# Kernel tuning notes

Measured on AMD Instinct MI355X. Metric: run time of the kernel, lower is better.

Reference implementation:

```python
import jax, jax.numpy as jnp
from jax import lax
import numpy as np


def _lstm_layer(x, Wih, Whh, bih, bhh):
    """Single-direction LSTM layer, PyTorch gate order (i, f, g, o).
    x: [B, T, D_in] -> hidden sequence [B, T, H]."""
    B, T, _ = x.shape
    H = Whh.shape[1]
    # Precompute input contribution for all timesteps: [B, T, 4H]
    xw = jnp.einsum('btd,gd->btg', x, Wih) + bih + bhh

    def step(carry, xt):
        h, c = carry
        gates = xt + h @ Whh.T  # [B, 4H]
        i, f, g, o = jnp.split(gates, 4, axis=-1)
        i = jax.nn.sigmoid(i)
        f = jax.nn.sigmoid(f)
        g = jnp.tanh(g)
        o = jax.nn.sigmoid(o)
        c = f * c + i * g
        h = o * jnp.tanh(c)
        return (h, c), h

    h0 = jnp.zeros((B, H), dtype=x.dtype)
    c0 = jnp.zeros((B, H), dtype=x.dtype)
    _, hs = lax.scan(step, (h0, c0), jnp.swapaxes(xw, 0, 1))  # [T, B, H]
    return jnp.swapaxes(hs, 0, 1)  # [B, T, H]


def setup_inputs() -> dict:
    key = jax.random.key(0)
    ks = jax.random.split(key, 9)
    B, T, D, H = 64, 2048, 256, 128
    s = 1.0 / np.sqrt(H)  # PyTorch uniform(-1/sqrt(H), 1/sqrt(H)) init scale
    u = lambda k, shp: jax.random.uniform(k, shp, jnp.float32, -s, s)
    return {
        'x': jax.random.normal(ks[0], (B, T, D), jnp.float32),
        'Wih0': u(ks[1], (4 * H, D)),
        'Whh0': u(ks[2], (4 * H, H)),
        'bih0': u(ks[3], (4 * H,)),
        'bhh0': u(ks[4], (4 * H,)),
        'Wih1': u(ks[5], (4 * H, H)),
        'Whh1': u(ks[6], (4 * H, H)),
        'bih1': u(ks[7], (4 * H,)),
        'bhh1': u(ks[8], (4 * H,)),
    }


def reference(x, Wih0, Whh0, bih0, bhh0, Wih1, Whh1, bih1, bhh1):
    # 2-layer stacked LSTM; inter-layer dropout (p=0.1) is identity at eval.
    h1 = _lstm_layer(x, Wih0, Whh0, bih0, bhh0)
    h2 = _lstm_layer(h1, Wih1, Whh1, bih1, bhh1)
    return h2
```

## Files before the change

### kernel.cpp

```cpp
#include <hip/hip_runtime.h>
#include <hip/hip_bf16.h>

#define H 128
#define FOURH 512
#define BATCH 64
#define SEQ 2048
#define TC SEQ
#define NCHUNK 128
#define NGEMMB 224

typedef _Float16 half8 __attribute__((ext_vector_type(8)));
typedef float f32x4 __attribute__((ext_vector_type(4)));

__global__ void prep_kernel(const float* __restrict__ Wih0,
                            const float* __restrict__ bih0, const float* __restrict__ bhh0,
                            const float* __restrict__ bih1, const float* __restrict__ bhh1,
                            float* __restrict__ Wt0,
                            float* __restrict__ b0, float* __restrict__ b1,
                            int* __restrict__ flags) {
    int id = blockIdx.x * 256 + threadIdx.x;
    const int N0 = 256 * 512;
    if (id < N0) {
        int k = id >> 9, n = id & 511;
        Wt0[id] = Wih0[n * 256 + k];
    } else if (id < N0 + 512) {
        int i = id - N0;
        b0[i] = bih0[i] + bhh0[i];
    } else if (id < N0 + 1024) {
        int i = id - (N0 + 512);
        b1[i] = bih1[i] + bhh1[i];
    } else if (id < N0 + 1024 + 8 + NCHUNK) {
        flags[id - (N0 + 1024)] = 0;
    }
}

__device__ __forceinline__ float sigmoid_f(float x) {
    return __builtin_amdgcn_rcpf(1.f + __expf(-x));
}
__device__ __forceinline__ float tanh_f(float x) {
    return 1.f - 2.f * __builtin_amdgcn_rcpf(__expf(2.f * x) + 1.f);
}

#define LDS_BARRIER()                                                \
    do {                                                             \
        asm volatile("s_waitcnt lgkmcnt(0)" ::: "memory");           \
        __builtin_amdgcn_s_barrier();                                \
        __builtin_amdgcn_sched_barrier(0);                           \
    } while (0)

#define BM 128
#define BN 128
#define BK 32

__global__ __launch_bounds__(512, 2) void lstm_fused_kernel(
    const float* __restrict__ x,
    const float* __restrict__ Wt0,
    const float* __restrict__ b0sum,
    float* __restrict__ G,
    const float* __restrict__ Whh0,
    const float* __restrict__ Wih1,
    const float* __restrict__ Whh1,
    const float* __restrict__ b1,
    _Float16* __restrict__ h1p,
    float* __restrict__ out,
    int* __restrict__ flags)
{
    const int tid = threadIdx.x;

    int* prodF     = flags;
    int* chunkDone = flags + 8;

    __shared__ _Float16 hbuf[2][8][136];
    __shared__ float As[BK][BM + 4];
    __shared__ float Bs[BK][BN];

    if (blockIdx.x >= 16) {
        const int j   = blockIdx.x - 16;
        const int sub = j & 31;
        const int cls = j >> 5;
        const int by  = sub >> 2;
        const int bx  = sub & 3;
        const int n0  = bx * BN;
        const int tm  = tid >> 5;
        const int tn  = tid & 31;

        int ar[2], aq[2], bkk[2], bq[2];
#pragma unroll
        for (int l = 0; l < 2; ++l) {
            int fidx = tid + l * 512;
            ar[l] = fidx >> 3; aq[l] = fidx & 7;
            bkk[l] = fidx >> 5; bq[l] = fidx & 31;
        }
        float4 bv = *(const float4*)&b0sum[n0 + tn * 4];

        for (int c = cls; c < NCHUNK; c += 7) {
            const float* aptr[2];
#pragma unroll
            for (int l = 0; l < 2; ++l) {
                int rl = by * BM + ar[l];
                int b = rl >> 4;
                int t = c * 16 + (rl & 15);
                aptr[l] = x + ((size_t)b * SEQ + t) * 256 + aq[l] * 4;
            }
            float acc[2][4][4];
#pragma unroll
            for (int rh = 0; rh < 2; ++rh)
#pragma unroll
                for (int i = 0; i < 4; ++i)
#pragma unroll
                    for (int jj = 0; jj < 4; ++jj) acc[rh][i][jj] = 0.f;

            for (int k0 = 0; k0 < 256; k0 += BK) {
                __syncthreads();
#pragma unroll
                for (int l = 0; l < 2; ++l) {
                    float4 v = *(const float4*)(aptr[l] + k0);
                    As[aq[l] * 4 + 0][ar[l]] = v.x;
                    As[aq[l] * 4 + 1][ar[l]] = v.y;
                    As[aq[l] * 4 + 2][ar[l]] = v.z;
                    As[aq[l] * 4 + 3][ar[l]] = v.w;
                }
#pragma unroll
                for (int l = 0; l < 2; ++l) {
                    float4 v = *(const float4*)(Wt0 + (size_t)(k0 + bkk[l]) * FOURH + n0 + bq[l] * 4);
                    *(float4*)&Bs[bkk[l]][bq[l] * 4] = v;
                }
                __syncthreads();
#pragma unroll
                for (int kk = 0; kk < BK; ++kk) {
                    float a[8], bb[4];
                    *(float4*)&a[0] = *(const float4*)&As[kk][tm * 4];
                    *(float4*)&a[4] = *(const float4*)&As[kk][64 + tm * 4];
                    *(float4*)&bb[0] = *(const float4*)&Bs[kk][tn * 4];
#pragma unroll
                    for (int rh = 0; rh < 2; ++rh)
#pragma unroll
                        for (int i = 0; i < 4; ++i)
#pragma unroll
                            for (int jj = 0; jj < 4; ++jj)
                                acc[rh][i][jj] = fmaf(a[rh * 4 + i], bb[jj], acc[rh][i][jj]);
                }
            }
#pragma unroll
            for (int rh = 0; rh < 2; ++rh)
#pragma unroll
                for (int i = 0; i < 4; ++i) {
                    int rl = by * BM + rh * 64 + tm * 4 + i;
                    int b = rl >> 4;
                    int t = c * 16 + (rl & 15);
                    float* gp = G + ((size_t)b * SEQ + t) * FOURH + n0 + tn * 4;
                    float4 o = make_float4(acc[rh][i][0] + bv.x, acc[rh][i][1] + bv.y,
                                           acc[rh][i][2] + bv.z, acc[rh][i][3] + bv.w);
                    *(float4*)gp = o;
                }
            __syncthreads();
            if (tid == 0) {
                __threadfence();
                __hip_atomic_fetch_add(&chunkDone[c], 1, __ATOMIC_RELEASE,
                                       __HIP_MEMORY_SCOPE_AGENT);
            }
        }
        return;
    }

    const int w  = tid >> 6;
    const int l  = tid & 63;
    const int li = l & 15;
    const int q  = l >> 4;
    const int u  = 16 * w + li;
    const int b0 = q * 2;
    const int ab = ((li >> 2) * 2) + (li & 1);

#define WAIT_FLAG(ptr, tgtv)                                                   \
    do {                                                                       \
        if (tid == 0) {                                                        \
            while (__hip_atomic_load((ptr), __ATOMIC_RELAXED,                  \
                                     __HIP_MEMORY_SCOPE_AGENT) < (tgtv))       \
                __builtin_amdgcn_s_sleep(4);                                   \
            (void)__hip_atomic_load((ptr), __ATOMIC_ACQUIRE,                   \
                                    __HIP_MEMORY_SCOPE_AGENT);                 \
        }                                                                      \
        __syncthreads();                                                       \
    } while (0)

    if (blockIdx.x < 8) {
        const int g = blockIdx.x;

        half8 Bf[4][4];
#pragma unroll
        for (int tl = 0; tl < 4; ++tl)
#pragma unroll
            for (int kf = 0; kf < 4; ++kf) {
                const float* wp = Whh0 + (size_t)(tl * 128 + u) * H + kf * 32 + q * 8;
                float4 v0 = *(const float4*)wp;
                float4 v1 = *(const float4*)(wp + 4);
                half8 b;
                b[0] = (_Float16)v0.x; b[1] = (_Float16)v0.y;
                b[2] = (_Float16)v0.z; b[3] = (_Float16)v0.w;
                b[4] = (_Float16)v1.x; b[5] = (_Float16)v1.y;
                b[6] = (_Float16)v1.z; b[7] = (_Float16)v1.w;
                Bf[tl][kf] = b;
            }

        float c0 = 0.f, c1 = 0.f, h0 = 0.f, h1v = 0.f;
        hbuf[0][b0][u]     = (_Float16)0.f;
        hbuf[0][b0 + 1][u] = (_Float16)0.f;

        const float* gb = G + (size_t)(8 * g) * TC * FOURH;
        const int voff0 = b0 * TC * FOURH + u;
        const int voff1 = (b0 + 1) * TC * FOURH + u;

        WAIT_FLAG(&chunkDone[0], 32);

        float G0[8], G1[8], G2[8], G3[8];
        const float* gld = gb;
#pragma unroll
        for (int tl = 0; tl < 4; ++tl) {
            G0[tl * 2 + 0] = gld[voff0 + tl * H];
            G0[tl * 2 + 1] = gld[voff1 + tl * H];
        }
        gld += FOURH;
#pragma unroll
        for (int tl = 0; tl < 4; ++tl) {
            G1[tl * 2 + 0] = gld[voff0 + tl * H];
            G1[tl * 2 + 1] = gld[voff1 + tl * H];
        }
        gld += FOURH;
#pragma unroll
        for (int tl = 0; tl < 4; ++tl) {
            G2[tl * 2 + 0] = gld[voff0 + tl * H];
            G2[tl * 2 + 1] = gld[voff1 + tl * H];
        }
        gld += FOURH;
#pragma unroll
        for (int tl = 0; tl < 4; ++tl) {
            G3[tl * 2 + 0] = gld[voff0 + tl * H];
            G3[tl * 2 + 1] = gld[voff1 + tl * H];
        }
        gld += FOURH;

        _Float16* php = h1p + (size_t)(8 * g + b0) * H + u;

#define P_STEP(PB, GR)                                                            \
    {                                                                             \
        half8 Afr[4];                                                             \
        _Pragma("unroll")                                                         \
        for (int kf = 0; kf < 4; ++kf)                                            \
            Afr[kf] = *(const half8*)&hbuf[PB][ab][kf * 32 + q * 8];              \
        f32x4 acc[4];                                                             \
        _Pragma("unroll")                                                         \
        for (int tl = 0; tl < 4; ++tl) {                                          \
            acc[tl][0] = GR[tl * 2 + 0]; acc[tl][1] = GR[tl * 2 + 1];             \
            acc[tl][2] = 0.f;            acc[tl][3] = 0.f;                        \
        }                                                                         \
        _Pragma("unroll")                                                         \
        for (int tl = 0; tl < 4; ++tl) {                                          \
            GR[tl * 2 + 0] = gld[voff0 + tl * H];                                 \
            GR[tl * 2 + 1] = gld[voff1 + tl * H];                                 \
        }                                                                         \
        gld += FOURH;                                                             \
        _Pragma("unroll")                                                         \
        for (int kf = 0; kf < 4; ++kf)                                            \
            _Pragma("unroll")                                                     \
            for (int tl = 0; tl < 4; ++tl)                                        \
                acc[tl] = __builtin_amdgcn_mfma_f32_16x16x32_f16(Afr[kf], Bf[tl][kf], acc[tl], 0, 0, 0); \
        {                                                                         \
            float ig = sigmoid_f(acc[0][0]);                                      \
            float fg = sigmoid_f(acc[1][0]);                                      \
            float gg = tanh_f(acc[2][0]);                                         \
            float og = sigmoid_f(acc[3][0]);                                      \
            c0 = fmaf(fg, c0, ig * gg);                                           \
            h0 = og * tanh_f(c0);                                                 \
            float ig1 = sigmoid_f(acc[0][1]);                                     \
            float fg1 = sigmoid_f(acc[1][1]);                                     \
            float gg1 = tanh_f(acc[2][1]);                                        \
            float og1 = sigmoid_f(acc[3][1]);                                     \
            c1 = fmaf(fg1, c1, ig1 * gg1);                                        \
            h1v = og1 * tanh_f(c1);                                               \
        }                                                                         \
        hbuf[PB ^ 1][b0][u]     = (_Float16)h0;                                   \
        hbuf[PB ^ 1][b0 + 1][u] = (_Float16)h1v;                                  \
        php[0]   = (_Float16)h0;                                                  \
        php[128] = (_Float16)h1v;                                                 \
        php += BATCH * H;                                                         \
        LDS_BARRIER();                                                            \
    }

        for (int s4 = 0; s4 < TC; s4 += 4) {
            if ((s4 & 15) == 0) {
                int k = (s4 >> 4) + 1;
                if (k > NCHUNK - 1) k = NCHUNK - 1;
                WAIT_FLAG(&chunkDone[k], 32);
            }
            P_STEP(0, G0)
            P_STEP(1, G1)
            P_STEP(0, G2)
            P_STEP(1, G3)
            if ((s4 & 31) == 28) {
                __threadfence();
                __syncthreads();
                if (tid == 0)
                    __hip_atomic_store(&prodF[g], s4 + 4, __ATOMIC_RELEASE,
                                       __HIP_MEMORY_SCOPE_AGENT);
            }
        }
#undef P_STEP
    } else {
        const int g = blockIdx.x - 8;

        half8 Bf[4][8];
#pragma unroll
        for (int tl = 0; tl < 4; ++tl)
#pragma unroll
            for (int kf = 0; kf < 8; ++kf) {
                const float* base = (kf < 4) ? Wih1 : Whh1;
                int kk = (kf & 3) * 32 + q * 8;
                const float* wp = base + (size_t)(tl * 128 + u) * H + kk;
                float4 v0 = *(const float4*)wp;
                float4 v1 = *(const float4*)(wp + 4);
                half8 b;
                b[0] = (_Float16)v0.x; b[1] = (_Float16)v0.y;
                b[2] = (_Float16)v0.z; b[3] = (_Float16)v0.w;
                b[4] = (_Float16)v1.x; b[5] = (_Float16)v1.y;
                b[6] = (_Float16)v1.z; b[7] = (_Float16)v1.w;
                Bf[tl][kf] = b;
            }

        float bv[4];
#pragma unroll
        for (int tl = 0; tl < 4; ++tl) bv[tl] = b1[tl * 128 + u];

        float c0 = 0.f, c1 = 0.f, h0, h1v;
        hbuf[0][b0][u]     = (_Float16)0.f;
        hbuf[0][b0 + 1][u] = (_Float16)0.f;

        const _Float16* h1pG = h1p + (size_t)(8 * g + ab) * H + q * 8;
        float* op0 = out + (size_t)(8 * g + b0) * SEQ * H + u;
        float* op1 = out + (size_t)(8 * g + b0 + 1) * SEQ * H + u;

        WAIT_FLAG(&prodF[g], 64);

        half8 Af0[4], Af1[4];
#pragma unroll
        for (int kf = 0; kf < 4; ++kf)
            Af0[kf] = *(const half8*)(h1pG + kf * 32);
        {
            const _Float16* hp = h1pG + (size_t)(BATCH * H);
#pragma unroll
            for (int kf = 0; kf < 4; ++kf)
                Af1[kf] = *(const half8*)(hp + kf * 32);
        }

#define C_STEP(S, PB, AfU)                                                        \
    {                                                                             \
        half8 Ah[4];                                                              \
        _Pragma("unroll")                                                         \
        for (int kf = 0; kf < 4; ++kf)                                            \
            Ah[kf] = *(const half8*)&hbuf[PB][ab][kf * 32 + q * 8];               \
        f32x4 acc[4];                                                             \
        _Pragma("unroll")                                                         \
        for (int tl = 0; tl < 4; ++tl) {                                          \
            acc[tl][0] = bv[tl]; acc[tl][1] = bv[tl];                             \
            acc[tl][2] = bv[tl]; acc[tl][3] = bv[tl];                             \
        }                                                                         \
        _Pragma("unroll")                                                         \
        for (int kf = 0; kf < 4; ++kf)                                            \
            _Pragma("unroll")                                                     \
            for (int tl = 0; tl < 4; ++tl)                                        \
                acc[tl] = __builtin_amdgcn_mfma_f32_16x16x32_f16(AfU[kf], Bf[tl][kf], acc[tl], 0, 0, 0); \
        {                                                                         \
            int sn = (S) + 2; if (sn > TC - 1) sn = TC - 1;                       \
            const _Float16* hp = h1pG + (size_t)sn * (BATCH * H);                 \
            _Pragma("unroll")                                                     \
            for (int kf = 0; kf < 4; ++kf)                                        \
                AfU[kf] = *(const half8*)(hp + kf * 32);                          \
        }                                                                         \
        _Pragma("unroll")                                                         \
        for (int kf = 0; kf < 4; ++kf)                                            \
            _Pragma("unroll")                                                     \
            for (int tl = 0; tl < 4; ++tl)                                        \
                acc[tl] = __builtin_amdgcn_mfma_f32_16x16x32_f16(Ah[kf], Bf[tl][kf + 4], acc[tl], 0, 0, 0); \
        {                                                                         \
            float ig = sigmoid_f(acc[0][0]);                                      \
            float fg = sigmoid_f(acc[1][0]);                                      \
            float gg = tanh_f(acc[2][0]);                                         \
            float og = sigmoid_f(acc[3][0]);                                      \
            c0 = fmaf(fg, c0, ig * gg);                                           \
            h0 = og * tanh_f(c0);                                                 \
            float ig1 = sigmoid_f(acc[0][1]);                                     \
            float fg1 = sigmoid_f(acc[1][1]);                                     \
            float gg1 = tanh_f(acc[2][1]);                                        \
            float og1 = sigmoid_f(acc[3][1]);                                     \
            c1 = fmaf(fg1, c1, ig1 * gg1);                                        \
            h1v = og1 * tanh_f(c1);                                               \
        }                                                                         \
        hbuf[PB ^ 1][b0][u]     = (_Float16)h0;                                   \
        hbuf[PB ^ 1][b0 + 1][u] = (_Float16)h1v;                                  \
        op0[0] = h0;                                                              \
        op1[0] = h1v;                                                             \
        op0 += H; op1 += H;                                                       \
        LDS_BARRIER();                                                            \
    }

        for (int s4 = 0; s4 < TC; s4 += 4) {
            if (s4 && (s4 & 31) == 0) {
                int tgt = s4 + 64; if (tgt > TC) tgt = TC;
                WAIT_FLAG(&prodF[g], tgt);
            }
            C_STEP(s4 + 0, 0, Af0)
            C_STEP(s4 + 1, 1, Af1)
            C_STEP(s4 + 2, 0, Af0)
            C_STEP(s4 + 3, 1, Af1)
        }
#undef C_STEP
    }
#undef WAIT_FLAG
}

extern "C" void kernel_launch(void* const* d_in, const int* in_sizes, int n_in,
                              void* d_out, int out_size, void* d_ws, size_t ws_size,
                              hipStream_t stream) {
    const float* x    = (const float*)d_in[0];
    const float* Wih0 = (const float*)d_in[1];
    const float* Whh0 = (const float*)d_in[2];
    const float* bih0 = (const float*)d_in[3];
    const float* bhh0 = (const float*)d_in[4];
    const float* Wih1 = (const float*)d_in[5];
    const float* Whh1 = (const float*)d_in[6];
    const float* bih1 = (const float*)d_in[7];
    const float* bhh1 = (const float*)d_in[8];
    float* out = (float*)d_out;

    char* ws = (char*)d_ws;
    size_t off = 0;
    auto carve = [&](size_t bytes) -> char* {
        char* p = ws + off;
        off += (bytes + 255) & ~(size_t)255;
        return p;
    };

    float*     Wt0   = (float*)carve(256 * 512 * 4);
    float*     b0v   = (float*)carve(512 * 4);
    float*     b1v   = (float*)carve(512 * 4);
    _Float16*  h1p   = (_Float16*)carve((size_t)SEQ * BATCH * H * 2);
    int*       flags = (int*)carve((8 + NCHUNK) * 4);
    float*     gbuf  = (float*)carve((size_t)BATCH * SEQ * FOURH * 4 + 16384);

    prep_kernel<<<517, 256, 0, stream>>>(Wih0, bih0, bhh0, bih1, bhh1, Wt0, b0v, b1v, flags);

    lstm_fused_kernel<<<240, 512, 0, stream>>>(x, Wt0, b0v, gbuf,
                                               Whh0, Wih1, Whh1, b1v,
                                               h1p, out, flags);
}
```

Measured before the change: 2.071 ms.

## Offload layer-1 input projection to separate MFMA blocks overlapping the recurrence

Adds a new block role that waits on layer-0 progress flags and computes h1·Wih1ᵀ + bias for 16-step chunks with f16 MFMA. It writes the result to a new gate buffer and signals per-chunk completion flags. The layer-1 recurrent blocks then do only the Whh1 MFMAs per step and prefetch the precomputed gates four steps ahead. The aim is to roughly halve the serial MFMA work on the critical path. Alongside this, Wih1 is pre-converted to f16 in the prep kernel, the layer-0 input GEMM blocks drop from 224 to 128, and the layer-0 producer publishes progress every 16 steps instead of 32. The new path only runs if the workspace can hold an extra full gate buffer; otherwise the old layer-1 path remains. It adds global traffic and extra inter-block flag synchronisation.

```diff
diff --git a/kernel.cpp b/kernel.cpp
--- a/kernel.cpp
+++ b/kernel.cpp
@@ -7,7 +7,7 @@
 #define SEQ 2048
 #define TC SEQ
 #define NCHUNK 128
-#define NGEMMB 224
+#define GSTRIDE (BATCH * FOURH)
 
 typedef _Float16 half8 __attribute__((ext_vector_type(8)));
 typedef float f32x4 __attribute__((ext_vector_type(4)));
@@ -15,8 +15,10 @@
 __global__ void prep_kernel(const float* __restrict__ Wih0,
                             const float* __restrict__ bih0, const float* __restrict__ bhh0,
                             const float* __restrict__ bih1, const float* __restrict__ bhh1,
+                            const float* __restrict__ Wih1,
                             float* __restrict__ Wt0,
                             float* __restrict__ b0, float* __restrict__ b1,
+                            _Float16* __restrict__ wt1h,
                             int* __restrict__ flags) {
     int id = blockIdx.x * 256 + threadIdx.x;
     const int N0 = 256 * 512;
@@ -29,8 +31,11 @@
     } else if (id < N0 + 1024) {
         int i = id - (N0 + 512);
         b1[i] = bih1[i] + bhh1[i];
-    } else if (id < N0 + 1024 + 8 + NCHUNK) {
-        flags[id - (N0 + 1024)] = 0;
+    } else if (id < N0 + 1024 + 65536) {
+        int i = id - (N0 + 1024);
+        wt1h[i] = (_Float16)Wih1[i];
+    } else if (id < N0 + 1024 + 65536 + 272) {
+        flags[id - (N0 + 1024 + 65536)] = 0;
     }
 }
 
@@ -58,21 +63,89 @@
     const float* __restrict__ b0sum,
     float* __restrict__ G,
     const float* __restrict__ Whh0,
-    const float* __restrict__ Wih1,
+    const _Float16* __restrict__ wt1h,
     const float* __restrict__ Whh1,
     const float* __restrict__ b1,
     _Float16* __restrict__ h1p,
+    float* __restrict__ g1r,
     float* __restrict__ out,
-    int* __restrict__ flags)
+    int* __restrict__ flags,
+    int g1mode)
 {
     const int tid = threadIdx.x;
 
     int* prodF     = flags;
-    int* chunkDone = flags + 8;
+    int* chunkDone = flags + 16;
+    int* g1Done    = flags + 144;
 
     __shared__ _Float16 hbuf[2][8][136];
     __shared__ float As[BK][BM + 4];
     __shared__ float Bs[BK][BN];
+
+    if (blockIdx.x >= 144) {
+        const int j   = blockIdx.x - 144;
+        const int sub = j & 31;
+        const int cls = j >> 5;
+        const int by  = sub >> 2;
+        const int bx  = sub & 3;
+        const int n0  = bx * BN;
+        const int wv  = tid >> 6;
+        const int l   = tid & 63;
+        const int li  = l & 15;
+        const int q   = l >> 4;
+        const int gb1 = 8 * by + wv;
+
+        float bv1g[8];
+#pragma unroll
+        for (int ct = 0; ct < 8; ++ct) bv1g[ct] = b1[n0 + ct * 16 + li];
+
+        for (int m = cls; m < NCHUNK; m += 2) {
+            if (tid == 0) {
+                while (__hip_atomic_load(&prodF[by], __ATOMIC_RELAXED,
+                                         __HIP_MEMORY_SCOPE_AGENT) < 16 * (m + 1))
+                    __builtin_amdgcn_s_sleep(4);
+                (void)__hip_atomic_load(&prodF[by], __ATOMIC_ACQUIRE,
+                                        __HIP_MEMORY_SCOPE_AGENT);
+            }
+            __syncthreads();
+
+            const int t0 = m * 16;
+            half8 Af[4];
+            const _Float16* ap = h1p + ((size_t)(t0 + li) * BATCH + gb1) * H + q * 8;
+#pragma unroll
+            for (int kf = 0; kf < 4; ++kf)
+                Af[kf] = *(const half8*)(ap + kf * 32);
+
+            f32x4 acc1[8];
+#pragma unroll
+            for (int ct = 0; ct < 8; ++ct) {
+                acc1[ct][0] = bv1g[ct]; acc1[ct][1] = bv1g[ct];
+                acc1[ct][2] = bv1g[ct]; acc1[ct][3] = bv1g[ct];
+            }
+#pragma unroll
+            for (int ct = 0; ct < 8; ++ct) {
+                const _Float16* wp = wt1h + (size_t)(n0 + ct * 16 + li) * H + q * 8;
+#pragma unroll
+                for (int kf = 0; kf < 4; ++kf) {
+                    half8 Bfr = *(const half8*)(wp + kf * 32);
+                    acc1[ct] = __builtin_amdgcn_mfma_f32_16x16x32_f16(Af[kf], Bfr, acc1[ct], 0, 0, 0);
+                }
+            }
+            const int srow = t0 + q * 4;
+#pragma unroll
+            for (int ct = 0; ct < 8; ++ct)
+#pragma unroll
+                for (int i = 0; i < 4; ++i)
+                    g1r[((size_t)(srow + i) * BATCH + gb1) * FOURH + n0 + ct * 16 + li] = acc1[ct][i];
+            __syncthreads();
+            if (tid == 0) {
+                __threadfence();
+                __hip_atomic_fetch_add(&g1Done[m], 1, __ATOMIC_RELEASE,
+                                       __HIP_MEMORY_SCOPE_AGENT);
+            }
+        }
+        return;
+    }
 
     if (blockIdx.x >= 16) {
         const int j   = blockIdx.x - 16;
@@ -86,21 +159,21 @@
 
         int ar[2], aq[2], bkk[2], bq[2];
 #pragma unroll
-        for (int l = 0; l < 2; ++l) {
-            int fidx = tid + l * 512;
-            ar[l] = fidx >> 3; aq[l] = fidx & 7;
-            bkk[l] = fidx >> 5; bq[l] = fidx & 31;
-        }
-        float4 bv = *(const float4*)&b0sum[n0 + tn * 4];
-
-        for (int c = cls; c < NCHUNK; c += 7) {
+        for (int l2 = 0; l2 < 2; ++l2) {
+            int fidx = tid + l2 * 512;
+            ar[l2] = fidx >> 3; aq[l2] = fidx & 7;
+            bkk[l2] = fidx >> 5; bq[l2] = fidx & 31;
+        }
+        float4 bvg = *(const float4*)&b0sum[n0 + tn * 4];
+
+        for (int idx = cls; idx < NCHUNK; idx += 4) {
             const float* aptr[2];
 #pragma unroll
-            for (int l = 0; l < 2; ++l) {
-                int rl = by * BM + ar[l];
+            for (int l2 = 0; l2 < 2; ++l2) {
+                int rl = by * BM + ar[l2];
                 int b = rl >> 4;
-                int t = c * 16 + (rl & 15);
-                aptr[l] = x + ((size_t)b * SEQ + t) * 256 + aq[l] * 4;
+                int t = idx * 16 + (rl & 15);
+                aptr[l2] = x + ((size_t)b * SEQ + t) * 256 + aq[l2] * 4;
             }
             float acc[2][4][4];
 #pragma unroll
@@ -113,17 +186,17 @@
             for (int k0 = 0; k0 < 256; k0 += BK) {
                 __syncthreads();
 #pragma unroll
-                for (int l = 0; l < 2; ++l) {
-                    float4 v = *(const float4*)(aptr[l] + k0);
-                    As[aq[l] * 4 + 0][ar[l]] = v.x;
-                    As[aq[l] * 4 + 1][ar[l]] = v.y;
-                    As[aq[l] * 4 + 2][ar[l]] = v.z;
-                    As[aq[l] * 4 + 3][ar[l]] = v.w;
+                for (int l2 = 0; l2 < 2; ++l2) {
+                    float4 v = *(const float4*)(aptr[l2] + k0);
+                    As[aq[l2] * 4 + 0][ar[l2]] = v.x;
+                    As[aq[l2] * 4 + 1][ar[l2]] = v.y;
+                    As[aq[l2] * 4 + 2][ar[l2]] = v.z;
+                    As[aq[l2] * 4 + 3][ar[l2]] = v.w;
                 }
 #pragma unroll
-                for (int l = 0; l < 2; ++l) {
-                    float4 v = *(const float4*)(Wt0 + (size_t)(k0 + bkk[l]) * FOURH + n0 + bq[l] * 4);
-                    *(float4*)&Bs[bkk[l]][bq[l] * 4] = v;
+                for (int l2 = 0; l2 < 2; ++l2) {
+                    float4 v = *(const float4*)(Wt0 + (size_t)(k0 + bkk[l2]) * FOURH + n0 + bq[l2] * 4);
+                    *(float4*)&Bs[bkk[l2]][bq[l2] * 4] = v;
                 }
                 __syncthreads();
 #pragma unroll
@@ -147,16 +220,16 @@
                 for (int i = 0; i < 4; ++i) {
                     int rl = by * BM + rh * 64 + tm * 4 + i;
                     int b = rl >> 4;
-                    int t = c * 16 + (rl & 15);
+                    int t = idx * 16 + (rl & 15);
                     float* gp = G + ((size_t)b * SEQ + t) * FOURH + n0 + tn * 4;
-                    float4 o = make_float4(acc[rh][i][0] + bv.x, acc[rh][i][1] + bv.y,
-                                           acc[rh][i][2] + bv.z, acc[rh][i][3] + bv.w);
+                    float4 o = make_float4(acc[rh][i][0] + bvg.x, acc[rh][i][1] + bvg.y,
+                                           acc[rh][i][2] + bvg.z, acc[rh][i][3] + bvg.w);
                     *(float4*)gp = o;
                 }
             __syncthreads();
             if (tid == 0) {
                 __threadfence();
-                __hip_atomic_fetch_add(&chunkDone[c], 1, __ATOMIC_RELEASE,
+                __hip_atomic_fetch_add(&chunkDone[idx], 1, __ATOMIC_RELEASE,
                                        __HIP_MEMORY_SCOPE_AGENT);
             }
         }
@@ -296,7 +369,7 @@
             P_STEP(1, G1)
             P_STEP(0, G2)
             P_STEP(1, G3)
-            if ((s4 & 31) == 28) {
+            if ((s4 & 15) == 12) {
                 __threadfence();
                 __syncthreads();
                 if (tid == 0)
@@ -305,17 +378,15 @@
             }
         }
 #undef P_STEP
-    } else {
+    } else if (g1mode) {
         const int g = blockIdx.x - 8;
 
-        half8 Bf[4][8];
+        half8 Bf[4][4];
 #pragma unroll
         for (int tl = 0; tl < 4; ++tl)
 #pragma unroll
-            for (int kf = 0; kf < 8; ++kf) {
-                const float* base = (kf < 4) ? Wih1 : Whh1;
-                int kk = (kf & 3) * 32 + q * 8;
-                const float* wp = base + (size_t)(tl * 128 + u) * H + kk;
+            for (int kf = 0; kf < 4; ++kf) {
+                const float* wp = Whh1 + (size_t)(tl * 128 + u) * H + kf * 32 + q * 8;
                 float4 v0 = *(const float4*)wp;
                 float4 v1 = *(const float4*)(wp + 4);
                 half8 b;
@@ -326,6 +397,117 @@
                 Bf[tl][kf] = b;
             }
 
+        float c0 = 0.f, c1 = 0.f, h0, h1v;
+        hbuf[0][b0][u]     = (_Float16)0.f;
+        hbuf[0][b0 + 1][u] = (_Float16)0.f;
+
+        const int boff0 = (8 * g + b0) * FOURH + u;
+        const int boff1 = boff0 + FOURH;
+        float* op0 = out + (size_t)(8 * g + b0) * SEQ * H + u;
+        float* op1 = out + (size_t)(8 * g + b0 + 1) * SEQ * H + u;
+
+        WAIT_FLAG(&prodF[g], 96);
+        WAIT_FLAG(&g1Done[0], 32);
+
+        float Ga[8], Gb[8], Gc[8], Gd[8];
+#pragma unroll
+        for (int tl = 0; tl < 4; ++tl) {
+            Ga[tl * 2 + 0] = g1r[(size_t)0 * GSTRIDE + boff0 + tl * H];
+            Ga[tl * 2 + 1] = g1r[(size_t)0 * GSTRIDE + boff1 + tl * H];
+            Gb[tl * 2 + 0] = g1r[(size_t)1 * GSTRIDE + boff0 + tl * H];
+            Gb[tl * 2 + 1] = g1r[(size_t)1 * GSTRIDE + boff1 + tl * H];
+            Gc[tl * 2 + 0] = g1r[(size_t)2 * GSTRIDE + boff0 + tl * H];
+            Gc[tl * 2 + 1] = g1r[(size_t)2 * GSTRIDE + boff1 + tl * H];
+            Gd[tl * 2 + 0] = g1r[(size_t)3 * GSTRIDE + boff0 + tl * H];
+            Gd[tl * 2 + 1] = g1r[(size_t)3 * GSTRIDE + boff1 + tl * H];
+        }
+
+#define C1_STEP(S, PB, GR)                                                        \
+    {                                                                             \
+        half8 Afr[4];                                                             \
+        _Pragma("unroll")                                                         \
+        for (int kf = 0; kf < 4; ++kf)                                            \
+            Afr[kf] = *(const half8*)&hbuf[PB][ab][kf * 32 + q * 8];              \
+        f32x4 acc[4];                                                             \
+        _Pragma("unroll")                                                         \
+        for (int tl = 0; tl < 4; ++tl) {                                          \
+            acc[tl][0] = GR[tl * 2 + 0]; acc[tl][1] = GR[tl * 2 + 1];             \
+            acc[tl][2] = 0.f;            acc[tl][3] = 0.f;                        \
+        }                                                                         \
+        {                                                                         \
+            const float* gp_ = g1r + (size_t)((S) + 4) * GSTRIDE;   \
+            _Pragma("unroll")                                                     \
+            for (int tl = 0; tl < 4; ++tl) {                                      \
+                GR[tl * 2 + 0] = gp_[boff0 + tl * H];                             \
+                GR[tl * 2 + 1] = gp_[boff1 + tl * H];                             \
+            }                                                                     \
+        }                                                                         \
+        _Pragma("unroll")                                                         \
+        for (int kf = 0; kf < 4; ++kf)                                            \
+            _Pragma("unroll")                                                     \
+            for (int tl = 0; tl < 4; ++tl)                                        \
+                acc[tl] = __builtin_amdgcn_mfma_f32_16x16x32_f16(Afr[kf], Bf[tl][kf], acc[tl], 0, 0, 0); \
+        {                                                                         \
+            float ig = sigmoid_f(acc[0][0]);                                      \
+            float fg = sigmoid_f(acc[1][0]);                                      \
+            float gg = tanh_f(acc[2][0]);                                         \
+            float og = sigmoid_f(acc[3][0]);                                      \
+            c0 = fmaf(fg, c0, ig * gg);                                           \
+            h0 = og * tanh_f(c0);                                                 \
+            float ig1 = sigmoid_f(acc[0][1]);                                     \
+            float fg1 = sigmoid_f(acc[1][1]);                                     \
+            float gg1 = tanh_f(acc[2][1]);                                        \
+            float og1 = sigmoid_f(acc[3][1]);                                     \
+            c1 = fmaf(fg1, c1, ig1 * gg1);                                        \
+            h1v = og1 * tanh_f(c1);                                               \
+        }                                                                         \
+        hbuf[PB ^ 1][b0][u]     = (_Float16)h0;                                   \
+        hbuf[PB ^ 1][b0 + 1][u] = (_Float16)h1v;                                  \
+        op0[0] = h0;                                                              \
+        op1[0] = h1v;                                                             \
+        op0 += H; op1 += H;                                                       \
+        LDS_BARRIER();                                                            \
+    }
+
+        for (int s4 = 0; s4 < TC; s4 += 4) {
+            if ((s4 & 15) == 0) {
+                int k = (s4 >> 4) + 1;
+                if (k > NCHUNK - 1) k = NCHUNK - 1;
+                WAIT_FLAG(&g1Done[k], 32);
+            }
+            C1_STEP(s4 + 0, 0, Ga)
+            C1_STEP(s4 + 1, 1, Gb)
+            C1_STEP(s4 + 2, 0, Gc)
+            C1_STEP(s4 + 3, 1, Gd)
+        }
+#undef C1_STEP
+    } else {
+        const int g = blockIdx.x - 8;
+
+        half8 Bf[4][8];
+#pragma unroll
+        for (int tl = 0; tl < 4; ++tl)
+#pragma unroll
+            for (int kf = 0; kf < 8; ++kf) {
+                const float* base = (kf < 4) ? (const float*)0 : Whh1;
+                int kk = (kf & 3) * 32 + q * 8;
+                half8 b;
+                if (kf < 4) {
+                    const _Float16* wp = wt1h + (size_t)(tl * 128 + u) * H + kk;
+                    b = *(const half8*)wp;
+                } else {
+                    const float* wp = Whh1 + (size_t)(tl * 128 + u) * H + kk;
+                    float4 v0 = *(const float4*)wp;
+                    float4 v1 = *(const float4*)(wp + 4);
+                    b[0] = (_Float16)v0.x; b[1] = (_Float16)v0.y;
+                    b[2] = (_Float16)v0.z; b[3] = (_Float16)v0.w;
+                    b[4] = (_Float16)v1.x; b[5] = (_Float16)v1.y;
+                    b[6] = (_Float16)v1.z; b[7] = (_Float16)v1.w;
+                }
+                (void)base;
+                Bf[tl][kf] = b;
+            }
+
         float bv[4];
 #pragma unroll
         for (int tl = 0; tl < 4; ++tl) bv[tl] = b1[tl * 128 + u];
@@ -351,7 +533,7 @@
                 Af1[kf] = *(const half8*)(hp + kf * 32);
         }
 
-#define C_STEP(S, PB, AfU)                                                        \
+#define C0_STEP(S, PB, AfU)                                                       \
     {                                                                             \
         half8 Ah[4];                                                              \
         _Pragma("unroll")                                                         \
@@ -407,12 +589,12 @@
                 int tgt = s4 + 64; if (tgt > TC) tgt = TC;
                 WAIT_FLAG(&prodF[g], tgt);
             }
-            C_STEP(s4 + 0, 0, Af0)
-            C_STEP(s4 + 1, 1, Af1)
-            C_STEP(s4 + 2, 0, Af0)
-            C_STEP(s4 + 3, 1, Af1)
-        }
-#undef C_STEP
+            C0_STEP(s4 + 0, 0, Af0)
+            C0_STEP(s4 + 1, 1, Af1)
+            C0_STEP(s4 + 2, 0, Af0)
+            C0_STEP(s4 + 3, 1, Af1)
+        }
+#undef C0_STEP
     }
 #undef WAIT_FLAG
 }
@@ -442,13 +624,20 @@
     float*     Wt0   = (float*)carve(256 * 512 * 4);
     float*     b0v   = (float*)carve(512 * 4);
     float*     b1v   = (float*)carve(512 * 4);
+    _Float16*  wt1h  = (_Float16*)carve(65536 * 2);
     _Float16*  h1p   = (_Float16*)carve((size_t)SEQ * BATCH * H * 2);
-    int*       flags = (int*)carve((8 + NCHUNK) * 4);
+    int*       flags = (int*)carve(272 * 4);
     float*     gbuf  = (float*)carve((size_t)BATCH * SEQ * FOURH * 4 + 16384);
 
-    prep_kernel<<<517, 256, 0, stream>>>(Wih0, bih0, bhh0, bih1, bhh1, Wt0, b0v, b1v, flags);
-
-    lstm_fused_kernel<<<240, 512, 0, stream>>>(x, Wt0, b0v, gbuf,
-                                               Whh0, Wih1, Whh1, b1v,
-                                               h1p, out, flags);
+    size_t g1bytes = (size_t)(SEQ + 8) * GSTRIDE * 4;
+    int g1mode = (off + g1bytes + 256) <= ws_size;
+    float* g1r = g1mode ? (float*)carve(g1bytes) : (float*)gbuf;
+
+    prep_kernel<<<774, 256, 0, stream>>>(Wih0, bih0, bhh0, bih1, bhh1, Wih1,
+                                         Wt0, b0v, b1v, wt1h, flags);
+
+    int nblocks = g1mode ? 208 : 144;
+    lstm_fused_kernel<<<nblocks, 512, 0, stream>>>(x, Wt0, b0v, gbuf,
+                                                   Whh0, wt1h, Whh1, b1v,
+                                                   h1p, g1r, out, flags, g1mode);
 }
```

Result: slower. 2.239 ms (+8.1%).
